# Kernel tuning notes

Measured on AMD Instinct MI355X. Metric: run time of the kernel, lower is better.

The kernel has to match this reference:

```python
import jax, jax.numpy as jnp
import numpy as np

# Config constants (match init_kwargs)
D_MODEL = 1024
N_EXPERTS = 8
EXPERT_SCALE = 2          # experts per base group -> n_base_groups = 4
N_FEAT = 16
BANK_DIM = 32
RAW_FEAT = N_FEAT * BANK_DIM   # 512
PROJ_DIM = 256
R_HIDDEN = 256
E_HIDDEN = 256
TOP_K = 2
TEMP = 1.0
LN_EPS = 1e-5


def _layernorm(x, g, b):
    mu = jnp.mean(x, axis=-1, keepdims=True)
    var = jnp.mean((x - mu) ** 2, axis=-1, keepdims=True)
    return (x - mu) * jax.lax.rsqrt(var + LN_EPS) * g + b


def _softmax_top_k(logits, k):
    # keep top-k logits, mask rest to -inf, softmax
    topv = jax.lax.top_k(logits, k)[0]
    thresh = topv[..., -1:]
    masked = jnp.where(logits >= thresh, logits, -jnp.inf)
    return jax.nn.softmax(masked, axis=-1)


def setup_inputs() -> dict:
    key = jax.random.key(0)
    ks = jax.random.split(key, 24)
    B, S = 4, 2048
    s = 0.02
    inp = {
        "hidden": jax.random.normal(ks[0], (B, S, D_MODEL), jnp.float32),
        "feat": jax.random.normal(ks[1], (B, S, N_FEAT), jnp.float32),
        "feat_bank": jax.random.normal(ks[2], (B, S, N_FEAT, BANK_DIM), jnp.float32),
        "item_seq_len": jax.random.randint(ks[3], (B,), 1, S + 1, jnp.int64),
        # pre-LN
        "ln_g": jnp.ones((D_MODEL,), jnp.float32),
        "ln_b": jnp.zeros((D_MODEL,), jnp.float32),
        # router feature projector (2 layers: Linear -> GELU -> Linear)
        "fp_w1": jax.random.normal(ks[4], (RAW_FEAT, PROJ_DIM), jnp.float32) * s,
        "fp_b1": jnp.zeros((PROJ_DIM,), jnp.float32),
        "fp_w2": jax.random.normal(ks[5], (PROJ_DIM, PROJ_DIM), jnp.float32) * s,
        "fp_b2": jnp.zeros((PROJ_DIM,), jnp.float32),
        # learned router MLP: d_in = d_model + proj_dim
        "r_w1": jax.random.normal(ks[6], (D_MODEL + PROJ_DIM, R_HIDDEN), jnp.float32) * s,
        "r_b1": jnp.zeros((R_HIDDEN,), jnp.float32),
        "r_w2": jax.random.normal(ks[7], (R_HIDDEN, N_EXPERTS), jnp.float32) * s,
        "r_b2": jnp.zeros((N_EXPERTS,), jnp.float32),
        # rule router (linear on raw stage features)
        "rr_w": jax.random.normal(ks[8], (N_FEAT, N_EXPERTS), jnp.float32) * s,
        "rr_b": jnp.zeros((N_EXPERTS,), jnp.float32),
        # per-expert FFN
        "e_w1": jax.random.normal(ks[9], (N_EXPERTS, D_MODEL, E_HIDDEN), jnp.float32) * s,
        "e_b1": jnp.zeros((N_EXPERTS, E_HIDDEN), jnp.float32),
        "e_w2": jax.random.normal(ks[10], (N_EXPERTS, E_HIDDEN, D_MODEL), jnp.float32) * s,
        "e_b2": jnp.zeros((N_EXPERTS, D_MODEL), jnp.float32),
        "alpha": jnp.ones((), jnp.float32),
    }
    return inp


def reference(hidden, feat, feat_bank, item_seq_len, ln_g, ln_b,
              fp_w1, fp_b1, fp_w2, fp_b2,
              r_w1, r_b1, r_w2, r_b2,
              rr_w, rr_b,
              e_w1, e_b1, e_w2, e_b2, alpha):
    B, S, D = hidden.shape
    h_norm = _layernorm(hidden, ln_g, ln_b)  # [B,S,D]

    # router feature path: flatten bank, 2-layer GELU projector
    bank_flat = feat_bank.reshape(B, S, RAW_FEAT)
    proj = jnp.dot(jax.nn.gelu(jnp.dot(bank_flat, fp_w1) + fp_b1), fp_w2) + fp_b2  # [B,S,P]

    # token-mode router input: concat hidden + projected features
    router_input = jnp.concatenate([h_norm, proj], axis=-1)
    rule_logits = jnp.dot(feat, rr_w) + rr_b  # rule router on raw stage features

    raw_logits = jnp.dot(jax.nn.gelu(jnp.dot(router_input, r_w1) + r_b1), r_w2) + r_b2
    scaled_logits = raw_logits / max(TEMP, 1e-6)
    gate_weights = _softmax_top_k(scaled_logits, TOP_K)           # [B,S,E]
    rule_target_logits = rule_logits / max(TEMP, 1e-6)

    # expert group: per-expert 2-layer GELU FFN on h_norm
    h1 = jax.nn.gelu(jnp.einsum('bsd,edh->bseh', h_norm, e_w1) + e_b1)
    expert_out = jnp.einsum('bseh,ehd->bsed', h1, e_w2) + e_b2    # [B,S,E,D]

    stage_out = jnp.einsum('bse,bsed->bsd', gate_weights, expert_out)
    next_hidden = hidden + alpha * stage_out

    # _aggregate_group_weights: expert_group_idx = arange(E)//EXPERT_SCALE is
    # contiguous, so gather+sum per group == reshape+sum over the scale axis
    n_groups = N_EXPERTS // EXPERT_SCALE
    group_weights = gate_weights.reshape(B, S, n_groups, EXPERT_SCALE).sum(-1)

    return (next_hidden, stage_out, gate_weights, scaled_logits, group_weights, rule_target_logits)
```

## Files before the change

### kernel.cpp

```cpp
#include <hip/hip_runtime.h>
#include <stdint.h>


typedef unsigned short u16;
using bf16x8 = __attribute__((ext_vector_type(8))) short;
using f32x4  = __attribute__((ext_vector_type(4))) float;

#define WS_HHI 0u
#define WS_HLO 16777216u
#define WS_PB2 33554432u
#define WS_W1T 67108864u
#define WS_IDX 71303168u
#define IX_SELE   0u
#define IX_SELG   65536u
#define IX_ROW    131072u
#define IX_TOKR   196608u
#define IX_GROW   262144u
#define IX_CNT    327680u
#define IX_CBASE  335872u
#define IX_TILEE  344064u
#define IX_TILES  344704u
#define IX_TILEC  345344u
#define IX_META   345984u
#define IX_TILEE2 346112u
#define IX_TILES2 347264u
#define IX_TILEC2 348416u

__device__ __forceinline__ float gelu_tanh(float x) {
  float x3 = x * x * x;
  float t = tanhf(0.7978845608028654f * (x + 0.044715f * x3));
  return 0.5f * x * (1.0f + t);
}
__device__ __forceinline__ u16 f2bf(float f) {
  uint32_t u = __float_as_uint(f);
  u = u + 0x7fffu + ((u >> 16) & 1u);
  return (u16)(u >> 16);
}
__device__ __forceinline__ float b2f(u16 h) {
  return __uint_as_float(((uint32_t)h) << 16);
}
__device__ __forceinline__ void gll16(const void* g, void* l) {
  __builtin_amdgcn_global_load_lds(
      (const __attribute__((address_space(1))) void*)g,
      (__attribute__((address_space(3))) void*)l, 16, 0, 0);
}

__global__ __launch_bounds__(256) void split_bank_kernel(const float* __restrict__ x,
    u16* __restrict__ hi, u16* __restrict__ lo) {
  int i4 = blockIdx.x * 256 + threadIdx.x;
  float4 v = ((const float4*)x)[i4];
  ushort4 h, l;
  h.x = f2bf(v.x); l.x = f2bf(v.x - b2f(h.x));
  h.y = f2bf(v.y); l.y = f2bf(v.y - b2f(h.y));
  h.z = f2bf(v.z); l.z = f2bf(v.z - b2f(h.z));
  h.w = f2bf(v.w); l.w = f2bf(v.w - b2f(h.w));
  ((ushort4*)hi)[i4] = h;
  ((ushort4*)lo)[i4] = l;
}

__global__ __launch_bounds__(256) void tsplit_kernel(const float* __restrict__ in,
    int inR, int inC, u16* __restrict__ outHi, u16* __restrict__ outLo,
    int outLD, int outColOff) {
  __shared__ u16 hs[64][65];
  __shared__ u16 ls[64][65];
  int tid = threadIdx.x;
  int c0 = blockIdx.x * 64, r0 = blockIdx.y * 64;
  const float* inp = in + (size_t)blockIdx.z * inR * inC;
  int rl = tid >> 6, cl = tid & 63;
#pragma unroll
  for (int p = 0; p < 16; p++) {
    int r = rl + p * 4;
    float v = inp[(size_t)(r0 + r) * inC + c0 + cl];
    u16 h = f2bf(v);
    hs[r][cl] = h;
    ls[r][cl] = f2bf(v - b2f(h));
  }
  __syncthreads();
  size_t obase = (size_t)(blockIdx.z * inC + c0) * outLD + outColOff + r0;
#pragma unroll
  for (int p = 0; p < 16; p++) {
    int c = rl + p * 4;
    outHi[obase + (size_t)c * outLD + cl] = hs[cl][c];
    if (outLo) outLo[obase + (size_t)c * outLD + cl] = ls[cl][c];
  }
}

__global__ __launch_bounds__(256) void wprime_kernel(const float* __restrict__ fp_w2,
    const float* __restrict__ r_w1, const float* __restrict__ fp_b2,
    const float* __restrict__ r_b1, float* __restrict__ wp, float* __restrict__ bp) {
  __shared__ float row[256];
  int i = blockIdx.x, n = threadIdx.x;
  if (i < 256) {
    row[n] = fp_w2[i * 256 + n];
    __syncthreads();
    float acc = 0.0f;
    for (int j = 0; j < 256; j++) acc += row[j] * r_w1[(size_t)(1024 + j) * 256 + n];
    wp[i * 256 + n] = acc;
  } else {
    row[n] = fp_b2[n];
    __syncthreads();
    float acc = r_b1[n];
    for (int j = 0; j < 256; j++) acc += row[j] * r_w1[(size_t)(1024 + j) * 256 + n];
    bp[n] = acc;
  }
}

__global__ __launch_bounds__(256) void ln_kernel(const float* __restrict__ hidden,
    const float* __restrict__ ln_g, const float* __restrict__ ln_b,
    const float* __restrict__ feat, const float* __restrict__ rr_w,
    const float* __restrict__ rr_b,
    u16* __restrict__ h_hi, u16* __restrict__ h_lo, float* __restrict__ rule) {
  int t = blockIdx.x;
  int tid = threadIdx.x;
  float4 v = ((const float4*)(hidden + (size_t)t * 1024))[tid];
  float s = v.x + v.y + v.z + v.w;
#pragma unroll
  for (int o = 32; o > 0; o >>= 1) s += __shfl_down(s, o);
  __shared__ float red[4];
  __shared__ float stats[2];
  int wid = tid >> 6, lane = tid & 63;
  if (lane == 0) red[wid] = s;
  __syncthreads();
  if (tid == 0) stats[0] = (red[0] + red[1] + red[2] + red[3]) * (1.0f / 1024.0f);
  __syncthreads();
  float mu = stats[0];
  float dx = v.x - mu, dy = v.y - mu, dz = v.z - mu, dw = v.w - mu;
  float q = dx * dx + dy * dy + dz * dz + dw * dw;
#pragma unroll
  for (int o = 32; o > 0; o >>= 1) q += __shfl_down(q, o);
  if (lane == 0) red[wid] = q;
  __syncthreads();
  if (tid == 0) {
    float var = (red[0] + red[1] + red[2] + red[3]) * (1.0f / 1024.0f) + 1e-5f;
    float r = rsqrtf(var);
    r = r * (1.5f - 0.5f * var * r * r);
    stats[1] = r;
  }
  __syncthreads();
  float r = stats[1];
  float4 g = ((const float4*)ln_g)[tid];
  float4 b = ((const float4*)ln_b)[tid];
  float4 o;
  o.x = dx * r * g.x + b.x;
  o.y = dy * r * g.y + b.y;
  o.z = dz * r * g.z + b.z;
  o.w = dw * r * g.w + b.w;
  ushort4 hv, lv;
  hv.x = f2bf(o.x); lv.x = f2bf(o.x - b2f(hv.x));
  hv.y = f2bf(o.y); lv.y = f2bf(o.y - b2f(hv.y));
  hv.z = f2bf(o.z); lv.z = f2bf(o.z - b2f(hv.z));
  hv.w = f2bf(o.w); lv.w = f2bf(o.w - b2f(hv.w));
  ((ushort4*)(h_hi + (size_t)t * 1024))[tid] = hv;
  ((ushort4*)(h_lo + (size_t)t * 1024))[tid] = lv;
  if (tid < 8) {
    float acc = rr_b[tid];
#pragma unroll
    for (int f = 0; f < 16; f++) acc += feat[t * 16 + f] * rr_w[f * 8 + tid];
    rule[t * 8 + tid] = acc;
  }
}

#define GF_COMPUTE(AH, AL, BH, BL)                                             \
  {                                                                            \
    bf16x8 afh[2], afl[2], bfh[2], bfl[2];                                     \
    _Pragma("unroll") for (int i = 0; i < 2; i++) {                            \
      afh[i] = *((const bf16x8*)(AH + (wr + i * 16 + l16) * 32 + xq * 8));     \
      afl[i] = *((const bf16x8*)(AL + (wr + i * 16 + l16) * 32 + xq * 8));     \
      bfh[i] = *((const bf16x8*)(BH + (wc + i * 16 + l16) * 32 + xq * 8));     \
      bfl[i] = *((const bf16x8*)(BL + (wc + i * 16 + l16) * 32 + xq * 8));     \
    }                                                                          \
    _Pragma("unroll") for (int i = 0; i < 2; i++)                              \
      _Pragma("unroll") for (int j = 0; j < 2; j++) {                          \
        acc[i][j] = __builtin_amdgcn_mfma_f32_16x16x32_bf16(afh[i], bfh[j], acc[i][j], 0, 0, 0); \
        acc[i][j] = __builtin_amdgcn_mfma_f32_16x16x32_bf16(afl[i], bfh[j], acc[i][j], 0, 0, 0); \
        acc[i][j] = __builtin_amdgcn_mfma_f32_16x16x32_bf16(afh[i], bfl[j], acc[i][j], 0, 0, 0); \
      }                                                                        \
  }

__global__ __launch_bounds__(256) void gfuse_kernel(
    const u16* __restrict__ A1h, const u16* __restrict__ A1l, int lda1, int klen1,
    const u16* __restrict__ A2h, const u16* __restrict__ A2l, int lda2, int klen2,
    const u16* __restrict__ Bth, const u16* __restrict__ Btl, int Kb,
    const float* __restrict__ bias,
    u16* __restrict__ outHi, u16* __restrict__ outLo, int fout) {
  __shared__ u16 Ash0[2048], Ash1[2048];
  __shared__ u16 Asl0[2048], Asl1[2048];
  __shared__ u16 Bsh0[2048], Bsh1[2048];
  __shared__ u16 Bsl0[2048], Bsl1[2048];
  int tid = threadIdx.x;
  int n = blockIdx.x;
  int rowt = ((n >> 5) << 3) + (n & 7);
  int cblk = (n >> 3) & 3;
  int row0 = rowt * 64, col0 = cblk * 64;
  int wave = tid >> 6, lane = tid & 63;
  int wr = (wave >> 1) * 32, wc = (wave & 1) * 32;
  int l16 = lane & 15, qd = lane >> 4;
  int xq = qd ^ ((l16 >> 1) & 3);
  f32x4 acc[2][2];
#pragma unroll
  for (int i = 0; i < 2; i++)
#pragma unroll
    for (int j = 0; j < 2; j++) acc[i][j] = 0.0f;

  int r0 = tid >> 2, kc = tid & 3;
  int kcs8 = (kc ^ ((r0 >> 1) & 3)) * 8;
  const u16* A1hp = A1h + (size_t)(row0 + r0) * lda1 + kcs8;
  const u16* A1lp = A1l + (size_t)(row0 + r0) * lda1 + kcs8;
  const u16* A2hp = A2h ? A2h + (size_t)(row0 + r0) * lda2 + kcs8 : (const u16*)0;
  const u16* A2lp = A2l ? A2l + (size_t)(row0 + r0) * lda2 + kcs8 : (const u16*)0;
  const u16* Bhp = Bth + (size_t)(col0 + r0) * Kb + kcs8;
  const u16* Blp = Btl + (size_t)(col0 + r0) * Kb + kcs8;
  int KT = klen1 + klen2;

#define GF_STAGE(K, AH, AL, BH, BL)                       \
  {                                                       \
    int kk = (K);                                         \
    if (kk < klen1) {                                     \
      gll16(A1hp + kk, AH + tid * 8);                     \
      gll16(A1lp + kk, AL + tid * 8);                     \
    } else {                                              \
      gll16(A2hp + (kk - klen1), AH + tid * 8);           \
      gll16(A2lp + (kk - klen1), AL + tid * 8);           \
    }                                                     \
    gll16(Bhp + kk, BH + tid * 8);                        \
    gll16(Blp + kk, BL + tid * 8);                        \
  }

  GF_STAGE(0, Ash0, Asl0, Bsh0, Bsl0);
  __syncthreads();
  for (int k0 = 0; k0 < KT; k0 += 64) {
    GF_STAGE(k0 + 32, Ash1, Asl1, Bsh1, Bsl1);
    GF_COMPUTE(Ash0, Asl0, Bsh0, Bsl0);
    __syncthreads();
    if (k0 + 64 < KT) {
      GF_STAGE(k0 + 64, Ash0, Asl0, Bsh0, Bsl0);
    }
    GF_COMPUTE(Ash1, Asl1, Bsh1, Bsl1);
    __syncthreads();
  }
#undef GF_STAGE

  if (fout) {
    float* of = (float*)outHi;
#pragma unroll
    for (int i = 0; i < 2; i++)
#pragma unroll
      for (int j = 0; j < 2; j++) {
        int cl = wc + j * 16 + l16;
        float bc = bias[col0 + cl];
#pragma unroll
        for (int rr = 0; rr < 4; rr++) {
          int rl = wr + i * 16 + qd * 4 + rr;
          of[(size_t)(row0 + rl) * 256 + col0 + cl] = gelu_tanh(acc[i][j][rr] + bc);
        }
      }
  } else {
#pragma unroll
    for (int i = 0; i < 2; i++)
#pragma unroll
      for (int j = 0; j < 2; j++) {
        int cl = wc + j * 16 + l16;
        float bc = bias[col0 + cl];
#pragma unroll
        for (int rr = 0; rr < 4; rr++) {
          int rl = wr + i * 16 + qd * 4 + rr;
          float v = gelu_tanh(acc[i][j][rr] + bc);
          u16 h = f2bf(v);
          size_t o = (size_t)(row0 + rl) * 256 + col0 + cl;
          outHi[o] = h;
          outLo[o] = f2bf(v - b2f(h));
        }
      }
  }
}

__global__ __launch_bounds__(256) void gate_kernel(const float* __restrict__ r1,
    const float* __restrict__ r_w2, const float* __restrict__ r_b2,
    float* __restrict__ gates, float* __restrict__ slog, float* __restrict__ gw,
    int* __restrict__ selE, float* __restrict__ selG, int* __restrict__ cnt) {
  __shared__ float w2s[2048];
  __shared__ float r1s[32][260];
  __shared__ float lg[32][8];
  __shared__ int se_s[64];
  int tid = threadIdx.x;
  int blk = blockIdx.x;
  int t0 = blk * 32;
  for (int i = tid; i < 2048; i += 256) {
    int e = i >> 8, k = i & 255;
    w2s[i] = r_w2[k * 8 + e];
  }
  for (int i = tid; i < 8192; i += 256) {
    int tt = i >> 8, k = i & 255;
    r1s[tt][k] = r1[(size_t)(t0 + tt) * 256 + k];
  }
  __syncthreads();
  {
    int tl = tid >> 3, e = tid & 7;
    float acc = r_b2[e];
    const float* wrp = &w2s[e * 256];
    const float* rrp = &r1s[tl][0];
    for (int k = 0; k < 256; k += 4) {
      float4 a = *(const float4*)(rrp + k);
      float4 b = *(const float4*)(wrp + k);
      acc += a.x * b.x + a.y * b.y + a.z * b.z + a.w * b.w;
    }
    lg[tl][e] = acc;
  }
  __syncthreads();
  if (tid < 32) {
    int t = t0 + tid;
    float l[8];
#pragma unroll
    for (int i = 0; i < 8; i++) l[i] = lg[tid][i];
    float m1 = -1e30f, m2 = -1e30f;
    int i1 = 0, i2 = 0;
#pragma unroll
    for (int i = 0; i < 8; i++) {
      float v = l[i];
      if (v > m1) { m2 = m1; i2 = i1; m1 = v; i1 = i; }
      else if (v > m2) { m2 = v; i2 = i; }
    }
    float w[8];
    float se = 0.0f;
#pragma unroll
    for (int i = 0; i < 8; i++) {
      float ex = (l[i] >= m2) ? expf(l[i] - m1) : 0.0f;
      w[i] = ex;
      se += ex;
    }
    float inv = 1.0f / se;
#pragma unroll
    for (int i = 0; i < 8; i++) {
      gates[(size_t)t * 8 + i] = w[i] * inv;
      slog[(size_t)t * 8 + i] = l[i];
    }
#pragma unroll
    for (int gi = 0; gi < 4; gi++)
      gw[(size_t)t * 4 + gi] = (w[2 * gi] + w[2 * gi + 1]) * inv;
    se_s[tid * 2] = i1;
    se_s[tid * 2 + 1] = i2;
    selE[t * 2] = i1;      selG[t * 2] = w[i1] * inv;
    selE[t * 2 + 1] = i2;  selG[t * 2 + 1] = w[i2] * inv;
  }
  __syncthreads();
  if (tid < 8) {
    int c = 0;
#pragma unroll
    for (int s = 0; s < 64; s++) c += (se_s[s] == tid) ? 1 : 0;
    cnt[blk * 8 + tid] = c;
  }
}

__global__ __launch_bounds__(256) void stageb_kernel(const int* __restrict__ cnt,
    int* __restrict__ cbase, int* __restrict__ tileE, int* __restrict__ tileS,
    int* __restrict__ tileC, int* __restrict__ tileE2, int* __restrict__ tileS2,
    int* __restrict__ tileC2, int* __restrict__ meta) {
  __shared__ int cs[2048];
  __shared__ int tot[8];
  __shared__ int ebase[8];
  int tid = threadIdx.x;
  for (int i = tid; i < 2048; i += 256) cs[i] = cnt[i];
  __syncthreads();
  if (tid < 8) {
    int s = 0;
    for (int c = 0; c < 256; c++) s += cs[c * 8 + tid];
    tot[tid] = s;
  }
  __syncthreads();
  if (tid == 0) {
    int b = 0, nt = 0;
    for (int e = 0; e < 8; e++) {
      ebase[e] = b;
      int c = tot[e];
      for (int off = 0; off < c; off += 128) {
        tileE[nt] = e; tileS[nt] = b + off;
        tileC[nt] = (c - off < 128) ? (c - off) : 128;
        nt++;
      }
      b += c;
    }
    meta[16] = nt;
    int b2 = 0, nt2 = 0;
    for (int e = 0; e < 8; e++) {
      int c = tot[e];
      for (int off = 0; off < c; off += 64) {
        tileE2[nt2] = e; tileS2[nt2] = b2 + off;
        tileC2[nt2] = (c - off < 64) ? (c - off) : 64;
        nt2++;
      }
      b2 += c;
    }
    meta[17] = nt2;
  }
  __syncthreads();
  if (tid < 8) {
    int run = ebase[tid];
    for (int c = 0; c < 256; c++) {
      cbase[c * 8 + tid] = run;
      run += cs[c * 8 + tid];
    }
  }
}

__global__ __launch_bounds__(256) void scatter_kernel(const int* __restrict__ selE,
    const float* __restrict__ selG, const int* __restrict__ cbase,
    int* __restrict__ rowsel, int* __restrict__ tokrow, float* __restrict__ grow) {
  int chunk = blockIdx.x;
  int wave = threadIdx.x >> 6, lane = threadIdx.x & 63;
  int slot = chunk * 64 + lane;
  int sel = selE[slot];
  float g = selG[slot];
  int tokn = chunk * 32 + (lane >> 1);
  unsigned long long lt = (1ULL << lane) - 1ULL;
#pragma unroll
  for (int ei = 0; ei < 2; ei++) {
    int e = wave + ei * 4;
    unsigned long long m = __ballot(sel == e);
    if (sel == e) {
      int row = cbase[chunk * 8 + e] + __popcll(m & lt);
      rowsel[slot] = row;
      tokrow[row] = tokn;
      grow[row] = g;
    }
  }
}

__global__ __launch_bounds__(256) void gexp1_kernel(const u16* __restrict__ A,
    const u16* __restrict__ w1t, const float* __restrict__ e_b1,
    const int* __restrict__ tokrow, const float* __restrict__ grow,
    const int* __restrict__ tileE2, const int* __restrict__ tileS2,
    const int* __restrict__ tileC2, const int* __restrict__ meta,
    u16* __restrict__ pb1) {
  __shared__ u16 As0[64 * 32];
  __shared__ u16 As1[64 * 32];
  __shared__ u16 Bs0[64 * 32];
  __shared__ u16 Bs1[64 * 32];
  __shared__ float gsl[64];
  int n = blockIdx.x;
  int ty = ((n >> 5) << 3) + (n & 7);
  int cblk = (n >> 3) & 3;
  if (ty >= meta[17]) return;
  int e = tileE2[ty], pstart = tileS2[ty], pcnt = tileC2[ty];
  int tid = threadIdx.x;
  int col0 = cblk * 64;
  if (tid < 64) {
    int rr = (tid < pcnt) ? tid : (pcnt - 1);
    gsl[tid] = grow[pstart + rr];
  }
  int wave = tid >> 6, lane = tid & 63;
  int wr = (wave >> 1) * 32, wc = (wave & 1) * 32;
  int l16 = lane & 15, qd = lane >> 4;
  int xq = qd ^ ((l16 >> 1) & 3);
  f32x4 acc[2][2];
  acc[0][0] = 0.0f; acc[0][1] = 0.0f; acc[1][0] = 0.0f; acc[1][1] = 0.0f;

  int r0 = tid >> 2, kc = tid & 3;
  int kcs = kc ^ ((r0 >> 1) & 3);
  int ra = (r0 < pcnt) ? r0 : (pcnt - 1);
  int ta = tokrow[pstart + ra];
  const u16* Ap = A + (size_t)ta * 1024 + kcs * 8;
  const u16* Bp = w1t + (size_t)(e * 256 + col0 + r0) * 1024 + kcs * 8;
  u16* dA0 = As0 + tid * 8;
  u16* dA1 = As1 + tid * 8;
  u16* dB0 = Bs0 + tid * 8;
  u16* dB1 = Bs1 + tid * 8;

  int aoff0 = (wr + l16) * 32 + xq * 8;
  int aoff1 = aoff0 + 16 * 32;
  int boff0 = (wc + l16) * 32 + xq * 8;
  int boff1 = boff0 + 16 * 32;

  gll16(Ap, dA0);
  gll16(Bp, dB0);
  __syncthreads();

  for (int k0 = 0; k0 < 1024; k0 += 64) {
    {
      gll16(Ap + k0 + 32, dA1);
      gll16(Bp + k0 + 32, dB1);
      bf16x8 a0 = *((const bf16x8*)(As0 + aoff0));
      bf16x8 a1 = *((const bf16x8*)(As0 + aoff1));
      bf16x8 b0 = *((const bf16x8*)(Bs0 + boff0));
      bf16x8 b1 = *((const bf16x8*)(Bs0 + boff1));
      acc[0][0] = __builtin_amdgcn_mfma_f32_16x16x32_bf16(a0, b0, acc[0][0], 0, 0, 0);
      acc[0][1] = __builtin_amdgcn_mfma_f32_16x16x32_bf16(a0, b1, acc[0][1], 0, 0, 0);
      acc[1][0] = __builtin_amdgcn_mfma_f32_16x16x32_bf16(a1, b0, acc[1][0], 0, 0, 0);
      acc[1][1] = __builtin_amdgcn_mfma_f32_16x16x32_bf16(a1, b1, acc[1][1], 0, 0, 0);
      __syncthreads();
    }
    {
      if (k0 + 64 < 1024) {
        gll16(Ap + k0 + 64, dA0);
        gll16(Bp + k0 + 64, dB0);
      }
      bf16x8 a0 = *((const bf16x8*)(As1 + aoff0));
      bf16x8 a1 = *((const bf16x8*)(As1 + aoff1));
      bf16x8 b0 = *((const bf16x8*)(Bs1 + boff0));
      bf16x8 b1 = *((const bf16x8*)(Bs1 + boff1));
      acc[0][0] = __builtin_amdgcn_mfma_f32_16x16x32_bf16(a0, b0, acc[0][0], 0, 0, 0);
      acc[0][1] = __builtin_amdgcn_mfma_f32_16x16x32_bf16(a0, b1, acc[0][1], 0, 0, 0);
      acc[1][0] = __builtin_amdgcn_mfma_f32_16x16x32_bf16(a1, b0, acc[1][0], 0, 0, 0);
      acc[1][1] = __builtin_amdgcn_mfma_f32_16x16x32_bf16(a1, b1, acc[1][1], 0, 0, 0);
      __syncthreads();
    }
  }

#pragma unroll
  for (int i = 0; i < 2; i++)
#pragma unroll
    for (int j = 0; j < 2; j++) {
      int cl = wc + j * 16 + l16;
      int col = col0 + cl;
      float bc = e_b1[e * 256 + col];
#pragma unroll
      for (int rr = 0; rr < 4; rr++) {
        int rl = wr + i * 16 + qd * 4 + rr;
        if (rl < pcnt) {
          float v = gelu_tanh(acc[i][j][rr] + bc) * gsl[rl];
          pb1[(size_t)(pstart + rl) * 256 + col] = f2bf(v);
        }
      }
    }
}

#define GX2_STAGE(K, AS, BS)              \
  gll16(Ap0 + (K), AS + tid * 8);         \
  gll16(Ap1 + (K), AS + tid * 8 + 2048);  \
  gll16(Bp0 + (K), BS + tid * 8);         \
  gll16(Bp1 + (K), BS + tid * 8 + 2048);

#define GX2_COMPUTE(AS, BS)                                                   \
  {                                                                           \
    bf16x8 af[4], bfr[4];                                                     \
    _Pragma("unroll") for (int i = 0; i < 4; i++) {                           \
      af[i]  = *((const bf16x8*)(AS + (wr + i * 16 + l16) * 32 + xq * 8));    \
      bfr[i] = *((const bf16x8*)(BS + (wc + i * 16 + l16) * 32 + xq * 8));    \
    }                                                                         \
    _Pragma("unroll") for (int i = 0; i < 4; i++)                             \
      _Pragma("unroll") for (int j = 0; j < 4; j++)                           \
        acc[i][j] = __builtin_amdgcn_mfma_f32_16x16x32_bf16(af[i], bfr[j], acc[i][j], 0, 0, 0); \
  }

__global__ __launch_bounds__(256) void gexp2_kernel(const u16* __restrict__ pb1,
    const u16* __restrict__ w2te,
    const int* __restrict__ tileE, const int* __restrict__ tileS,
    const int* __restrict__ tileC, const int* __restrict__ meta,
    u16* __restrict__ pb2) {
  int ty = blockIdx.y;
  if (ty >= meta[16]) return;
  int e = tileE[ty], pstart = tileS[ty], pcnt = tileC[ty];
  if (pcnt <= 0) return;
  __shared__ u16 As0[4096], As1[4096];
  __shared__ u16 Bs0[4096], Bs1[4096];
  int tid = threadIdx.x;
  int col0 = blockIdx.x * 128;
  int wave = tid >> 6, lane = tid & 63;
  int wr = (wave >> 1) * 64, wc = (wave & 1) * 64;
  int l16 = lane & 15, qd = lane >> 4;
  int xq = qd ^ ((l16 >> 1) & 3);
  f32x4 acc[4][4];
#pragma unroll
  for (int i = 0; i < 4; i++)
#pragma unroll
    for (int j = 0; j < 4; j++) acc[i][j] = 0.0f;

  int r0 = tid >> 2, kc = tid & 3;
  int kcs = kc ^ ((r0 >> 1) & 3);
  int ra = (r0 < pcnt) ? r0 : (pcnt - 1);
  int rb = (r0 + 64 < pcnt) ? (r0 + 64) : (pcnt - 1);
  const u16* Ap0 = pb1 + (size_t)(pstart + ra) * 256 + kcs * 8;
  const u16* Ap1 = pb1 + (size_t)(pstart + rb) * 256 + kcs * 8;
  const u16* Bp0 = w2te + (size_t)(e * 1024 + col0 + r0) * 256 + kcs * 8;
  const u16* Bp1 = Bp0 + (size_t)64 * 256;

  GX2_STAGE(0, As0, Bs0);
  __syncthreads();
  for (int k0 = 0; k0 < 256; k0 += 64) {
    GX2_STAGE(k0 + 32, As1, Bs1);
    GX2_COMPUTE(As0, Bs0);
    __syncthreads();
    if (k0 + 64 < 256) {
      GX2_STAGE(k0 + 64, As0, Bs0);
    }
    GX2_COMPUTE(As1, Bs1);
    __syncthreads();
  }

#pragma unroll
  for (int i = 0; i < 4; i++)
#pragma unroll
    for (int j = 0; j < 4; j++) {
      int cl = wc + j * 16 + l16;
#pragma unroll
      for (int rr = 0; rr < 4; rr++) {
        int rl = wr + i * 16 + qd * 4 + rr;
        if (rl < pcnt)
          pb2[(size_t)(pstart + rl) * 1024 + col0 + cl] = f2bf(acc[i][j][rr]);
      }
    }
}

__global__ __launch_bounds__(256) void combine_kernel(const u16* __restrict__ pb2,
    const int* __restrict__ rowsel, const int* __restrict__ selE,
    const float* __restrict__ selG, const float* __restrict__ e_b2,
    const float* __restrict__ hidden, const float* __restrict__ alpha_p,
    float* __restrict__ stage, float* __restrict__ next) {
  int t = blockIdx.x;
  int c = threadIdx.x * 4;
  int rA = rowsel[t * 2], rB = rowsel[t * 2 + 1];
  int eA = selE[t * 2], eB = selE[t * 2 + 1];
  float gA = selG[t * 2], gB = selG[t * 2 + 1];
  float al = alpha_p[0];
  ushort4 pa = *((const ushort4*)(pb2 + (size_t)rA * 1024 + c));
  ushort4 pb = *((const ushort4*)(pb2 + (size_t)rB * 1024 + c));
  float4 ba = *((const float4*)(e_b2 + (size_t)eA * 1024 + c));
  float4 bb = *((const float4*)(e_b2 + (size_t)eB * 1024 + c));
  float4 h = *((const float4*)(hidden + (size_t)t * 1024 + c));
  float4 v;
  v.x = b2f(pa.x) + b2f(pb.x) + gA * ba.x + gB * bb.x;
  v.y = b2f(pa.y) + b2f(pb.y) + gA * ba.y + gB * bb.y;
  v.z = b2f(pa.z) + b2f(pb.z) + gA * ba.z + gB * bb.z;
  v.w = b2f(pa.w) + b2f(pb.w) + gA * ba.w + gB * bb.w;
  *((float4*)(stage + (size_t)t * 1024 + c)) = v;
  float4 n;
  n.x = h.x + al * v.x; n.y = h.y + al * v.y;
  n.z = h.z + al * v.z; n.w = h.w + al * v.w;
  *((float4*)(next + (size_t)t * 1024 + c)) = n;
}

extern "C" void kernel_launch(void* const* d_in, const int* in_sizes, int n_in,
                              void* d_out, int out_size, void* d_ws, size_t ws_size,
                              hipStream_t stream) {
  const float* hidden    = (const float*)d_in[0];
  const float* feat      = (const float*)d_in[1];
  const float* feat_bank = (const float*)d_in[2];
  const float* ln_g  = (const float*)d_in[4];
  const float* ln_b  = (const float*)d_in[5];
  const float* fp_w1 = (const float*)d_in[6];
  const float* fp_b1 = (const float*)d_in[7];
  const float* fp_w2 = (const float*)d_in[8];
  const float* fp_b2 = (const float*)d_in[9];
  const float* r_w1  = (const float*)d_in[10];
  const float* r_b1  = (const float*)d_in[11];
  const float* r_w2  = (const float*)d_in[12];
  const float* r_b2  = (const float*)d_in[13];
  const float* rr_w  = (const float*)d_in[14];
  const float* rr_b  = (const float*)d_in[15];
  const float* e_w1  = (const float*)d_in[16];
  const float* e_b1  = (const float*)d_in[17];
  const float* e_w2  = (const float*)d_in[18];
  const float* e_b2  = (const float*)d_in[19];
  const float* alpha = (const float*)d_in[20];

  char* ob = (char*)d_out;
  float* next  = (float*)ob;
  float* stage = (float*)(ob + 33554432);
  float* gates = (float*)(ob + 67108864);
  float* slog  = gates + 65536;
  float* gw    = slog + 65536;
  float* rule  = gw + 32768;

  u16* bank_hi  = (u16*)ob;
  u16* bank_lo  = (u16*)(ob + 8388608);
  float* r1     = (float*)ob;
  u16* fpw1t_hi = (u16*)(ob + 16777216);
  u16* fpw1t_lo = (u16*)(ob + 17039360);
  float* wp     = (float*)(ob + 17301504);
  float* bp     = (float*)(ob + 17563648);
  u16* rw1t_hi  = (u16*)(ob + 17825792);
  u16* rw1t_lo  = (u16*)(ob + 18481152);
  u16* mid_hi   = (u16*)(ob + 19136512);
  u16* mid_lo   = (u16*)(ob + 23330816);
  u16* w2te     = (u16*)(ob + 19136512);

  char* sb = ob + 33554432;
  u16* pb1     = (u16*)sb;

  char* ws = (char*)d_ws;
  u16* h_hi = (u16*)(ws + WS_HHI);
  u16* h_lo = (u16*)(ws + WS_HLO);
  u16* pb2  = (u16*)(ws + WS_PB2);
  u16* w1t  = (u16*)(ws + WS_W1T);
  char* ix  = ws + WS_IDX;
  int*   selE   = (int*)(ix + IX_SELE);
  float* selG   = (float*)(ix + IX_SELG);
  int*   rowsel = (int*)(ix + IX_ROW);
  int*   tokrow = (int*)(ix + IX_TOKR);
  float* grow   = (float*)(ix + IX_GROW);
  int*   cnt    = (int*)(ix + IX_CNT);
  int*   cbase  = (int*)(ix + IX_CBASE);
  int*   tileE  = (int*)(ix + IX_TILEE);
  int*   tileS  = (int*)(ix + IX_TILES);
  int*   tileC  = (int*)(ix + IX_TILEC);
  int*   tileE2 = (int*)(ix + IX_TILEE2);
  int*   tileS2 = (int*)(ix + IX_TILES2);
  int*   tileC2 = (int*)(ix + IX_TILEC2);
  int*   meta   = (int*)(ix + IX_META);

  split_bank_kernel<<<4096, 256, 0, stream>>>(feat_bank, bank_hi, bank_lo);
  wprime_kernel<<<257, 256, 0, stream>>>(fp_w2, r_w1, fp_b2, r_b1, wp, bp);
  tsplit_kernel<<<dim3(4, 8, 1), 256, 0, stream>>>(fp_w1, 512, 256,
      fpw1t_hi, fpw1t_lo, 512, 0);
  tsplit_kernel<<<dim3(4, 16, 1), 256, 0, stream>>>(r_w1, 1024, 256,
      rw1t_hi, rw1t_lo, 1280, 0);
  tsplit_kernel<<<dim3(4, 4, 1), 256, 0, stream>>>(wp, 256, 256,
      rw1t_hi, rw1t_lo, 1280, 1024);
  tsplit_kernel<<<dim3(4, 16, 8), 256, 0, stream>>>(e_w1, 1024, 256,
      w1t, nullptr, 1024, 0);
  ln_kernel<<<8192, 256, 0, stream>>>(hidden, ln_g, ln_b, feat, rr_w, rr_b,
                                      h_hi, h_lo, rule);
  gfuse_kernel<<<512, 256, 0, stream>>>(
      bank_hi, bank_lo, 512, 512,
      nullptr, nullptr, 0, 0,
      fpw1t_hi, fpw1t_lo, 512, fp_b1, mid_hi, mid_lo, 0);
  gfuse_kernel<<<512, 256, 0, stream>>>(
      h_hi, h_lo, 1024, 1024,
      mid_hi, mid_lo, 256, 256,
      rw1t_hi, rw1t_lo, 1280, bp, (u16*)r1, nullptr, 1);
  tsplit_kernel<<<dim3(16, 4, 8), 256, 0, stream>>>(e_w2, 256, 1024,
      w2te, nullptr, 256, 0);
  gate_kernel<<<256, 256, 0, stream>>>(r1, r_w2, r_b2, gates, slog, gw,
      selE, selG, cnt);
  stageb_kernel<<<1, 256, 0, stream>>>(cnt, cbase, tileE, tileS, tileC,
      tileE2, tileS2, tileC2, meta);
  scatter_kernel<<<256, 256, 0, stream>>>(selE, selG, cbase, rowsel, tokrow, grow);
  gexp1_kernel<<<1152, 256, 0, stream>>>(h_hi, w1t, e_b1, tokrow, grow,
      tileE2, tileS2, tileC2, meta, pb1);
  gexp2_kernel<<<dim3(8, 136), 256, 0, stream>>>(pb1, w2te, tileE, tileS, tileC,
      meta, pb2);
  combine_kernel<<<8192, 256, 0, stream>>>(pb2, rowsel, selE, selG, e_b2,
      hidden, alpha, stage, next);
}
```

Before: 338.8 us.

## Fuse bank bf16 split into GEMM and router second layer into GEMM epilogue

Removes the separate split_bank kernel: the bank GEMM now loads fp32 feat_bank directly and splits it into hi/lo bf16 while staging to LDS. The router GEMM no longer writes the fp32 r1 hidden activations. Instead its epilogue computes per-column-block partial logits against r_w2, and the gate kernel sums the four partials. This saves a 16MB read+write round trip plus the r1 write/read, at the cost of synchronous fp32 loads in the bank GEMM staging and extra LDS use in the router kernel.

```diff
diff --git a/kernel.cpp b/kernel.cpp
--- a/kernel.cpp
+++ b/kernel.cpp
@@ -25,6 +25,7 @@
 #define IX_TILEE2 346112u
 #define IX_TILES2 347264u
 #define IX_TILEC2 348416u
+#define IX_PLOG   1048576u
 
 __device__ __forceinline__ float gelu_tanh(float x) {
   float x3 = x * x * x;
@@ -43,19 +44,6 @@
   __builtin_amdgcn_global_load_lds(
       (const __attribute__((address_space(1))) void*)g,
       (__attribute__((address_space(3))) void*)l, 16, 0, 0);
-}
-
-__global__ __launch_bounds__(256) void split_bank_kernel(const float* __restrict__ x,
-    u16* __restrict__ hi, u16* __restrict__ lo) {
-  int i4 = blockIdx.x * 256 + threadIdx.x;
-  float4 v = ((const float4*)x)[i4];
-  ushort4 h, l;
-  h.x = f2bf(v.x); l.x = f2bf(v.x - b2f(h.x));
-  h.y = f2bf(v.y); l.y = f2bf(v.y - b2f(h.y));
-  h.z = f2bf(v.z); l.z = f2bf(v.z - b2f(h.z));
-  h.w = f2bf(v.w); l.w = f2bf(v.w - b2f(h.w));
-  ((ushort4*)hi)[i4] = h;
-  ((ushort4*)lo)[i4] = l;
 }
 
 __global__ __launch_bounds__(256) void tsplit_kernel(const float* __restrict__ in,
@@ -177,12 +165,11 @@
       }                                                                        \
   }
 
-__global__ __launch_bounds__(256) void gfuse_kernel(
-    const u16* __restrict__ A1h, const u16* __restrict__ A1l, int lda1, int klen1,
-    const u16* __restrict__ A2h, const u16* __restrict__ A2l, int lda2, int klen2,
-    const u16* __restrict__ Bth, const u16* __restrict__ Btl, int Kb,
+__global__ __launch_bounds__(256) void gfuse_bank_kernel(
+    const float* __restrict__ Af,
+    const u16* __restrict__ Bth, const u16* __restrict__ Btl,
     const float* __restrict__ bias,
-    u16* __restrict__ outHi, u16* __restrict__ outLo, int fout) {
+    u16* __restrict__ outHi, u16* __restrict__ outLo) {
   __shared__ u16 Ash0[2048], Ash1[2048];
   __shared__ u16 Asl0[2048], Asl1[2048];
   __shared__ u16 Bsh0[2048], Bsh1[2048];
@@ -197,114 +184,165 @@
   int l16 = lane & 15, qd = lane >> 4;
   int xq = qd ^ ((l16 >> 1) & 3);
   f32x4 acc[2][2];
+  acc[0][0] = 0.0f; acc[0][1] = 0.0f; acc[1][0] = 0.0f; acc[1][1] = 0.0f;
+
+  int r0 = tid >> 2, kc = tid & 3;
+  int sph8 = (kc ^ ((r0 >> 1) & 3)) * 8;
+  const float* Ap = Af + (size_t)(row0 + r0) * 512 + kc * 8;
+  const u16* Bhp = Bth + (size_t)(col0 + r0) * 512 + sph8;
+  const u16* Blp = Btl + (size_t)(col0 + r0) * 512 + sph8;
+  int aw = r0 * 32 + sph8;
+
+  union U8 { ushort u[8]; bf16x8 v; };
+
+#define GFB_STAGE(K, AH, AL, BH, BL)                                  \
+  {                                                                   \
+    gll16(Bhp + (K), BH + tid * 8);                                   \
+    gll16(Blp + (K), BL + tid * 8);                                   \
+    float4 va = *(const float4*)(Ap + (K));                           \
+    float4 vb = *(const float4*)(Ap + (K) + 4);                       \
+    float fv[8] = {va.x, va.y, va.z, va.w, vb.x, vb.y, vb.z, vb.w};   \
+    U8 H, L;                                                          \
+    _Pragma("unroll") for (int q = 0; q < 8; q++) {                   \
+      H.u[q] = f2bf(fv[q]);                                           \
+      L.u[q] = f2bf(fv[q] - b2f(H.u[q]));                             \
+    }                                                                 \
+    *(bf16x8*)(AH + aw) = H.v;                                        \
+    *(bf16x8*)(AL + aw) = L.v;                                        \
+  }
+
+  GFB_STAGE(0, Ash0, Asl0, Bsh0, Bsl0);
+  __syncthreads();
+  for (int k0 = 0; k0 < 512; k0 += 64) {
+    GFB_STAGE(k0 + 32, Ash1, Asl1, Bsh1, Bsl1);
+    GF_COMPUTE(Ash0, Asl0, Bsh0, Bsl0);
+    __syncthreads();
+    if (k0 + 64 < 512) {
+      GFB_STAGE(k0 + 64, Ash0, Asl0, Bsh0, Bsl0);
+    }
+    GF_COMPUTE(Ash1, Asl1, Bsh1, Bsl1);
+    __syncthreads();
+  }
+#undef GFB_STAGE
+
 #pragma unroll
   for (int i = 0; i < 2; i++)
 #pragma unroll
-    for (int j = 0; j < 2; j++) acc[i][j] = 0.0f;
+    for (int j = 0; j < 2; j++) {
+      int cl = wc + j * 16 + l16;
+      float bc = bias[col0 + cl];
+#pragma unroll
+      for (int rr = 0; rr < 4; rr++) {
+        int rl = wr + i * 16 + qd * 4 + rr;
+        float v = gelu_tanh(acc[i][j][rr] + bc);
+        u16 h = f2bf(v);
+        size_t o = (size_t)(row0 + rl) * 256 + col0 + cl;
+        outHi[o] = h;
+        outLo[o] = f2bf(v - b2f(h));
+      }
+    }
+}
+
+__global__ __launch_bounds__(256) void gfuse_router_kernel(
+    const u16* __restrict__ A1h, const u16* __restrict__ A1l,
+    const u16* __restrict__ A2h, const u16* __restrict__ A2l,
+    const u16* __restrict__ Bth, const u16* __restrict__ Btl,
+    const float* __restrict__ bias, const float* __restrict__ r_w2,
+    float* __restrict__ plog) {
+  __shared__ u16 Ash0[2048], Ash1[2048];
+  __shared__ u16 Asl0[2048], Asl1[2048];
+  __shared__ u16 Bsh0[2048], Bsh1[2048];
+  __shared__ u16 Bsl0[2048], Bsl1[2048];
+  __shared__ float r1s[64][65];
+  __shared__ float w2s[64][8];
+  int tid = threadIdx.x;
+  int n = blockIdx.x;
+  int rowt = ((n >> 5) << 3) + (n & 7);
+  int cblk = (n >> 3) & 3;
+  int row0 = rowt * 64, col0 = cblk * 64;
+  int wave = tid >> 6, lane = tid & 63;
+  int wr = (wave >> 1) * 32, wc = (wave & 1) * 32;
+  int l16 = lane & 15, qd = lane >> 4;
+  int xq = qd ^ ((l16 >> 1) & 3);
+  f32x4 acc[2][2];
+  acc[0][0] = 0.0f; acc[0][1] = 0.0f; acc[1][0] = 0.0f; acc[1][1] = 0.0f;
 
   int r0 = tid >> 2, kc = tid & 3;
   int kcs8 = (kc ^ ((r0 >> 1) & 3)) * 8;
-  const u16* A1hp = A1h + (size_t)(row0 + r0) * lda1 + kcs8;
-  const u16* A1lp = A1l + (size_t)(row0 + r0) * lda1 + kcs8;
-  const u16* A2hp = A2h ? A2h + (size_t)(row0 + r0) * lda2 + kcs8 : (const u16*)0;
-  const u16* A2lp = A2l ? A2l + (size_t)(row0 + r0) * lda2 + kcs8 : (const u16*)0;
-  const u16* Bhp = Bth + (size_t)(col0 + r0) * Kb + kcs8;
-  const u16* Blp = Btl + (size_t)(col0 + r0) * Kb + kcs8;
-  int KT = klen1 + klen2;
-
-#define GF_STAGE(K, AH, AL, BH, BL)                       \
+  const u16* A1hp = A1h + (size_t)(row0 + r0) * 1024 + kcs8;
+  const u16* A1lp = A1l + (size_t)(row0 + r0) * 1024 + kcs8;
+  const u16* A2hp = A2h + (size_t)(row0 + r0) * 256 + kcs8;
+  const u16* A2lp = A2l + (size_t)(row0 + r0) * 256 + kcs8;
+  const u16* Bhp = Bth + (size_t)(col0 + r0) * 1280 + kcs8;
+  const u16* Blp = Btl + (size_t)(col0 + r0) * 1280 + kcs8;
+
+#define GFR_STAGE(K, AH, AL, BH, BL)                      \
   {                                                       \
     int kk = (K);                                         \
-    if (kk < klen1) {                                     \
+    if (kk < 1024) {                                      \
       gll16(A1hp + kk, AH + tid * 8);                     \
       gll16(A1lp + kk, AL + tid * 8);                     \
     } else {                                              \
-      gll16(A2hp + (kk - klen1), AH + tid * 8);           \
-      gll16(A2lp + (kk - klen1), AL + tid * 8);           \
+      gll16(A2hp + (kk - 1024), AH + tid * 8);            \
+      gll16(A2lp + (kk - 1024), AL + tid * 8);            \
     }                                                     \
     gll16(Bhp + kk, BH + tid * 8);                        \
     gll16(Blp + kk, BL + tid * 8);                        \
   }
 
-  GF_STAGE(0, Ash0, Asl0, Bsh0, Bsl0);
-  __syncthreads();
-  for (int k0 = 0; k0 < KT; k0 += 64) {
-    GF_STAGE(k0 + 32, Ash1, Asl1, Bsh1, Bsl1);
+  GFR_STAGE(0, Ash0, Asl0, Bsh0, Bsl0);
+  __syncthreads();
+  for (int k0 = 0; k0 < 1280; k0 += 64) {
+    GFR_STAGE(k0 + 32, Ash1, Asl1, Bsh1, Bsl1);
     GF_COMPUTE(Ash0, Asl0, Bsh0, Bsl0);
     __syncthreads();
-    if (k0 + 64 < KT) {
-      GF_STAGE(k0 + 64, Ash0, Asl0, Bsh0, Bsl0);
+    if (k0 + 64 < 1280) {
+      GFR_STAGE(k0 + 64, Ash0, Asl0, Bsh0, Bsl0);
     }
     GF_COMPUTE(Ash1, Asl1, Bsh1, Bsl1);
     __syncthreads();
   }
-#undef GF_STAGE
-
-  if (fout) {
-    float* of = (float*)outHi;
-#pragma unroll
-    for (int i = 0; i < 2; i++)
-#pragma unroll
-      for (int j = 0; j < 2; j++) {
-        int cl = wc + j * 16 + l16;
-        float bc = bias[col0 + cl];
-#pragma unroll
-        for (int rr = 0; rr < 4; rr++) {
-          int rl = wr + i * 16 + qd * 4 + rr;
-          of[(size_t)(row0 + rl) * 256 + col0 + cl] = gelu_tanh(acc[i][j][rr] + bc);
-        }
+#undef GFR_STAGE
+
+#pragma unroll
+  for (int i = 0; i < 2; i++)
+#pragma unroll
+    for (int j = 0; j < 2; j++) {
+      int cl = wc + j * 16 + l16;
+      float bc = bias[col0 + cl];
+#pragma unroll
+      for (int rr = 0; rr < 4; rr++) {
+        int rl = wr + i * 16 + qd * 4 + rr;
+        r1s[rl][cl] = gelu_tanh(acc[i][j][rr] + bc);
       }
-  } else {
-#pragma unroll
-    for (int i = 0; i < 2; i++)
-#pragma unroll
-      for (int j = 0; j < 2; j++) {
-        int cl = wc + j * 16 + l16;
-        float bc = bias[col0 + cl];
-#pragma unroll
-        for (int rr = 0; rr < 4; rr++) {
-          int rl = wr + i * 16 + qd * 4 + rr;
-          float v = gelu_tanh(acc[i][j][rr] + bc);
-          u16 h = f2bf(v);
-          size_t o = (size_t)(row0 + rl) * 256 + col0 + cl;
-          outHi[o] = h;
-          outLo[o] = f2bf(v - b2f(h));
-        }
-      }
-  }
-}
-
-__global__ __launch_bounds__(256) void gate_kernel(const float* __restrict__ r1,
-    const float* __restrict__ r_w2, const float* __restrict__ r_b2,
+    }
+  for (int i = tid; i < 512; i += 256)
+    w2s[i >> 3][i & 7] = r_w2[(size_t)(col0 + (i >> 3)) * 8 + (i & 7)];
+  __syncthreads();
+#pragma unroll
+  for (int t2 = 0; t2 < 2; t2++) {
+    int idx = tid + t2 * 256;
+    int tok = idx >> 3, e = idx & 7;
+    float L = 0.0f;
+#pragma unroll
+    for (int c = 0; c < 64; c++) L += r1s[tok][c] * w2s[c][e];
+    plog[(size_t)(row0 + tok) * 32 + cblk * 8 + e] = L;
+  }
+}
+
+__global__ __launch_bounds__(256) void gate_kernel(const float* __restrict__ plog,
+    const float* __restrict__ r_b2,
     float* __restrict__ gates, float* __restrict__ slog, float* __restrict__ gw,
     int* __restrict__ selE, float* __restrict__ selG, int* __restrict__ cnt) {
-  __shared__ float w2s[2048];
-  __shared__ float r1s[32][260];
   __shared__ float lg[32][8];
   __shared__ int se_s[64];
   int tid = threadIdx.x;
   int blk = blockIdx.x;
   int t0 = blk * 32;
-  for (int i = tid; i < 2048; i += 256) {
-    int e = i >> 8, k = i & 255;
-    w2s[i] = r_w2[k * 8 + e];
-  }
-  for (int i = tid; i < 8192; i += 256) {
-    int tt = i >> 8, k = i & 255;
-    r1s[tt][k] = r1[(size_t)(t0 + tt) * 256 + k];
-  }
-  __syncthreads();
   {
     int tl = tid >> 3, e = tid & 7;
-    float acc = r_b2[e];
-    const float* wrp = &w2s[e * 256];
-    const float* rrp = &r1s[tl][0];
-    for (int k = 0; k < 256; k += 4) {
-      float4 a = *(const float4*)(rrp + k);
-      float4 b = *(const float4*)(wrp + k);
-      acc += a.x * b.x + a.y * b.y + a.z * b.z + a.w * b.w;
-    }
-    lg[tl][e] = acc;
+    const float* pp = plog + (size_t)(t0 + tl) * 32 + e;
+    lg[tl][e] = r_b2[e] + pp[0] + pp[8] + pp[16] + pp[24];
   }
   __syncthreads();
   if (tid < 32) {
@@ -660,9 +698,6 @@
   float* gw    = slog + 65536;
   float* rule  = gw + 32768;
 
-  u16* bank_hi  = (u16*)ob;
-  u16* bank_lo  = (u16*)(ob + 8388608);
-  float* r1     = (float*)ob;
   u16* fpw1t_hi = (u16*)(ob + 16777216);
   u16* fpw1t_lo = (u16*)(ob + 17039360);
   float* wp     = (float*)(ob + 17301504);
@@ -696,8 +731,8 @@
   int*   tileS2 = (int*)(ix + IX_TILES2);
   int*   tileC2 = (int*)(ix + IX_TILEC2);
   int*   meta   = (int*)(ix + IX_META);
-
-  split_bank_kernel<<<4096, 256, 0, stream>>>(feat_bank, bank_hi, bank_lo);
+  float* plog   = (float*)(ix + IX_PLOG);
+
   wprime_kernel<<<257, 256, 0, stream>>>(fp_w2, r_w1, fp_b2, r_b1, wp, bp);
   tsplit_kernel<<<dim3(4, 8, 1), 256, 0, stream>>>(fp_w1, 512, 256,
       fpw1t_hi, fpw1t_lo, 512, 0);
@@ -709,17 +744,14 @@
       w1t, nullptr, 1024, 0);
   ln_kernel<<<8192, 256, 0, stream>>>(hidden, ln_g, ln_b, feat, rr_w, rr_b,
                                       h_hi, h_lo, rule);
-  gfuse_kernel<<<512, 256, 0, stream>>>(
-      bank_hi, bank_lo, 512, 512,
-      nullptr, nullptr, 0, 0,
-      fpw1t_hi, fpw1t_lo, 512, fp_b1, mid_hi, mid_lo, 0);
-  gfuse_kernel<<<512, 256, 0, stream>>>(
-      h_hi, h_lo, 1024, 1024,
-      mid_hi, mid_lo, 256, 256,
-      rw1t_hi, rw1t_lo, 1280, bp, (u16*)r1, nullptr, 1);
+  gfuse_bank_kernel<<<512, 256, 0, stream>>>(
+      feat_bank, fpw1t_hi, fpw1t_lo, fp_b1, mid_hi, mid_lo);
+  gfuse_router_kernel<<<512, 256, 0, stream>>>(
+      h_hi, h_lo, mid_hi, mid_lo,
+      rw1t_hi, rw1t_lo, bp, r_w2, plog);
   tsplit_kernel<<<dim3(16, 4, 8), 256, 0, stream>>>(e_w2, 256, 1024,
       w2te, nullptr, 256, 0);
-  gate_kernel<<<256, 256, 0, stream>>>(r1, r_w2, r_b2, gates, slog, gw,
+  gate_kernel<<<256, 256, 0, stream>>>(plog, r_b2, gates, slog, gw,
       selE, selG, cnt);
   stageb_kernel<<<1, 256, 0, stream>>>(cnt, cbase, tileE, tileS, tileC,
       tileE2, tileS2, tileC2, meta);
```

Result: no change. 336.9 us (-0.6%).
